# Kernel optimization log

Measured on AMD Instinct MI355X. Metric: run time of the kernel, lower is better.

## Reference

```python
import jax, jax.numpy as jnp
import numpy as np

N, E, D, H, L = 20000, 100000, 768, 8, 3
DH = D // H
WSCALE = 0.02  # small init so exp() in attention stays finite


def setup_inputs() -> dict:
    key = jax.random.key(0)
    ks = jax.random.split(key, 16)
    inp = {
        'x': jax.random.normal(ks[0], (N, D), jnp.float32),
        'edge_attr': jax.random.normal(ks[1], (E, D), jnp.float32),
        'Wck': jax.random.normal(ks[2], (L, 2 * D, D), jnp.float32) * WSCALE,
        'bck': jnp.zeros((L, D), jnp.float32),
        'Wq': jax.random.normal(ks[3], (L, D, D), jnp.float32) * WSCALE,
        'bq': jnp.zeros((L, D), jnp.float32),
        'Wv': jax.random.normal(ks[4], (L, D, D), jnp.float32) * WSCALE,
        'bv': jnp.zeros((L, D), jnp.float32),
        'Waw': jax.random.normal(ks[5], (L, H, H), jnp.float32) * WSCALE,
        'baw': jnp.zeros((L, H), jnp.float32),
        'Wc': jax.random.normal(ks[6], (L, D, D), jnp.float32) * WSCALE,
        'bc': jnp.zeros((L, D), jnp.float32),
        'Wlx': jax.random.normal(ks[7], (L, D, D), jnp.float32) * WSCALE,
        'blx': jnp.zeros((L, D), jnp.float32),
        'Wla1': jax.random.normal(ks[8], (L, 2 * D, D), jnp.float32) * WSCALE,
        'bla1': jnp.zeros((L, D), jnp.float32),
        'Wla2': jax.random.normal(ks[9], (L, D, 2), jnp.float32) * WSCALE,
        'bla2': jnp.zeros((L, 2), jnp.float32),
        'edge_index': jax.random.randint(ks[10], (2, E), 0, N, jnp.int64),
    }
    return inp


def _gnn_layer(x, edge_attr, src, dst, Wck, bck, Wq, bq, Wv, bv, Waw, baw,
               Wc, bc, Wlx, blx, Wla1, bla1, Wla2, bla2):
    n = x.shape[0]
    # per-edge query (target node) and key (edge_attr || source node)
    q = x[dst] @ Wq + bq                                        # [E, D]
    k = jnp.concatenate([edge_attr, x[src]], axis=1) @ Wck + bck  # [E, D]
    qh = q.reshape(-1, H, DH)
    kh = k.reshape(-1, H, DH)
    aw = jnp.einsum('ehd,ehd->eh', qh, kh) / jnp.sqrt(jnp.float32(D))  # [E, H]
    a = jnp.exp(jax.nn.leaky_relu(aw, 0.2) @ Waw + baw)          # [E, H]
    # GAT-style softmax normalization over incoming edges of each target node
    sc = jax.ops.segment_sum(a, dst, num_segments=n)             # [N, H]
    ad = sc[dst]
    ad = jnp.where(ad == 0, jnp.float32(1), ad)
    att = (a / ad)[:, :, None]                                   # [E, H, 1]
    # weighted message from source nodes, scattered to targets
    v = (x[src] @ Wv + bv).reshape(-1, H, DH)                    # [E, H, DH]
    msg = (att * v).reshape(-1, D) @ Wc + bc                     # [E, D]
    h = jax.ops.segment_sum(msg, dst, num_segments=n)            # [N, D]
    # sgnn gated residual combine
    lx = x @ Wlx + blx
    z = jax.nn.leaky_relu(jnp.concatenate([lx, h], axis=1) @ Wla1 + bla1, 0.2) @ Wla2 + bla2
    la = jax.nn.softmax(z, axis=1)                               # [N, 2]
    return x * la[:, 0:1] + h * la[:, 1:2]


def reference(x, edge_attr, Wck, bck, Wq, bq, Wv, bv, Waw, baw, Wc, bc,
              Wlx, blx, Wla1, bla1, Wla2, bla2, edge_index):
    src = edge_index[0]
    dst = edge_index[1]
    for l in range(L):
        x = _gnn_layer(x, edge_attr, src, dst,
                       Wck[l], bck[l], Wq[l], bq[l], Wv[l], bv[l],
                       Waw[l], baw[l], Wc[l], bc[l], Wlx[l], blx[l],
                       Wla1[l], bla1[l], Wla2[l], bla2[l])
    return x
```

## Files before the change

### kernel.cpp

```cpp
#include <hip/hip_runtime.h>
#include <hip/hip_bf16.h>
#include <math.h>

#define DD 768
#define HH 8
#define DHH 96
#define NL 3
#define NN 20000
#define EE 100000

typedef __attribute__((ext_vector_type(8))) __bf16 bf16x8;
typedef __attribute__((ext_vector_type(4))) float f32x4;
typedef __attribute__((ext_vector_type(8))) unsigned short u16x8;

__host__ __device__ static inline int imin(int a, int b) { return a < b ? a : b; }

__device__ inline float b2f(unsigned short u) {
    union { unsigned int v; float f; } x; x.v = ((unsigned int)u) << 16; return x.f;
}
__device__ inline unsigned short f2b_rne(float f) {
    union { float f; unsigned int v; } x; x.f = f;
    unsigned int v = x.v;
    return (unsigned short)((v + 0x7FFFu + ((v >> 16) & 1u)) >> 16);
}
__device__ inline void b2f2(unsigned int u, float& lo, float& hi) {
    union { unsigned int v; float f; } x;
    x.v = u << 16; lo = x.f;
    x.v = u & 0xffff0000u; hi = x.f;
}
__device__ inline unsigned int packbf(float a, float b) {
    return (unsigned int)f2b_rne(a) | ((unsigned int)f2b_rne(b) << 16);
}

__global__ void deg_kernel(const int* __restrict__ dst, int* __restrict__ cnt)
{
    int i = blockIdx.x * 256 + threadIdx.x;
    if (i < EE) atomicAdd(&cnt[dst[i]], 1);
}

__global__ __launch_bounds__(256)
void scan_kernel(const int* __restrict__ deg, int* __restrict__ rowptr, int* __restrict__ cursor)
{
    __shared__ int part[256];
    int t = threadIdx.x;
    const int per = (NN + 255) / 256;
    int lo = t * per, hi = imin(NN, lo + per);
    int s = 0;
    for (int i = lo; i < hi; i++) s += deg[i];
    part[t] = s;
    __syncthreads();
    if (t == 0) {
        int acc = 0;
        for (int i = 0; i < 256; i++) { int v = part[i]; part[i] = acc; acc += v; }
        rowptr[NN] = acc;
    }
    __syncthreads();
    int run = part[t];
    for (int i = lo; i < hi; i++) {
        rowptr[i] = run; cursor[i] = run;
        run += deg[i];
    }
}

__global__ void fill_perm(const int* __restrict__ src, const int* __restrict__ dst,
                          int* __restrict__ cursor, int* __restrict__ perm,
                          int* __restrict__ src_s)
{
    int e = blockIdx.x * 256 + threadIdx.x;
    if (e >= EE) return;
    int d = dst[e];
    int pos = atomicAdd(&cursor[d], 1);
    perm[pos] = e;
    src_s[pos] = src[e];
}

__global__ void degf_kernel(const int* __restrict__ rowptr, float* __restrict__ degf)
{
    int n = blockIdx.x * 256 + threadIdx.x;
    if (n < NN) degf[n] = (float)(rowptr[n + 1] - rowptr[n]);
}

__global__ void f2b_kernel(const float* __restrict__ in, unsigned short* __restrict__ out, int n8)
{
    int i = blockIdx.x * 256 + threadIdx.x;
    if (i >= n8) return;
    const float4* p = reinterpret_cast<const float4*>(in + (size_t)i * 8);
    float4 a = p[0], b = p[1];
    u16x8 o;
    o[0] = f2b_rne(a.x); o[1] = f2b_rne(a.y); o[2] = f2b_rne(a.z); o[3] = f2b_rne(a.w);
    o[4] = f2b_rne(b.x); o[5] = f2b_rne(b.y); o[6] = f2b_rne(b.z); o[7] = f2b_rne(b.w);
    *reinterpret_cast<u16x8*>(out + (size_t)i * 8) = o;
}

__global__ void f2b_gather(const float* __restrict__ in, const int* __restrict__ perm,
                           unsigned short* __restrict__ out)
{
    int i = blockIdx.x * 256 + threadIdx.x;
    if (i >= EE * 96) return;
    int m = i / 96;
    int d8 = (i % 96) * 8;
    int row = perm[m];
    const float4* p = reinterpret_cast<const float4*>(in + (size_t)row * DD + d8);
    float4 a = p[0], b = p[1];
    u16x8 o;
    o[0] = f2b_rne(a.x); o[1] = f2b_rne(a.y); o[2] = f2b_rne(a.z); o[3] = f2b_rne(a.w);
    o[4] = f2b_rne(b.x); o[5] = f2b_rne(b.y); o[6] = f2b_rne(b.z); o[7] = f2b_rne(b.w);
    *reinterpret_cast<u16x8*>(out + (size_t)m * DD + d8) = o;
}

__global__ void transpose_w(const float* __restrict__ W, unsigned short* __restrict__ Wt,
                            int Kin, int out_ld, int out_off,
                            size_t strideW, size_t strideWt)
{
    __shared__ float tile[32][33];
    int z = blockIdx.z;
    W  += (size_t)z * strideW;
    Wt += (size_t)z * strideWt;
    int kb = blockIdx.x * 32, nb = blockIdx.y * 32;
    int tx = threadIdx.x & 31, ty = threadIdx.x >> 5;
#pragma unroll
    for (int i = 0; i < 32; i += 8)
        tile[ty + i][tx] = W[(size_t)(kb + ty + i) * DD + nb + tx];
    __syncthreads();
#pragma unroll
    for (int i = 0; i < 32; i += 8)
        Wt[(size_t)(nb + ty + i) * out_ld + out_off + kb + tx] = f2b_rne(tile[tx][ty + i]);
}

__global__ void biasf_kernel(const float* __restrict__ blx, const float* __restrict__ Wla1,
                             const float* __restrict__ bla1, float* __restrict__ bf)
{
    int l = blockIdx.y;
    const float* blxl  = blx  + (size_t)l * DD;
    const float* Wla1l = Wla1 + (size_t)l * 2 * DD * DD;
    const float* bla1l = bla1 + (size_t)l * DD;
    float* bfl = bf + (size_t)l * DD;
    int n = blockIdx.x * 256 + threadIdx.x;
    if (n >= DD) return;
    float s = bla1l[n];
    for (int k = 0; k < DD; k++) s += blxl[k] * Wla1l[(size_t)k * DD + n];
    bfl[n] = s;
}

__global__ void biasqkv_kernel(const float* __restrict__ bq, const float* __restrict__ bv,
                               float* __restrict__ bqkv)
{
    int l = blockIdx.y;
    int i = blockIdx.x * 256 + threadIdx.x;
    if (i >= 3 * DD) return;
    float v = 0.f;
    if (i < DD) v = bq[(size_t)l * DD + i];
    else if (i >= 2 * DD) v = bv[(size_t)l * DD + i - 2 * DD];
    bqkv[(size_t)l * 3 * DD + i] = v;
}

__global__ __launch_bounds__(512, 2)
void gemm_mfma(const unsigned short* __restrict__ A0,
               const unsigned short* __restrict__ A1,
               const unsigned short* __restrict__ Wt,
               const float* __restrict__ bias,
               const float* __restrict__ rowscale,
               float* __restrict__ C32,
               unsigned short* __restrict__ C16,
               int M, int K, int Nw,
               size_t bsA, size_t bsW, size_t bsC)
{
    __shared__ __align__(16) char smem[98304];
    const int z = blockIdx.z;
    A0 += (size_t)z * bsA;
    Wt += (size_t)z * bsW;
    if (C32) C32 += (size_t)z * bsC;
    if (C16) C16 += (size_t)z * bsC;
    const int t = threadIdx.x;
    const int l = t & 63;
    const int w = t >> 6;
    const int wm = w & 3, wn = w >> 2;

    const int gx = gridDim.x;
    const int nwg = gx * gridDim.y;
    const int lin = blockIdx.y * gx + blockIdx.x;
    const int xcd = lin & 7, pos = lin >> 3;
    const int q8 = nwg >> 3, r8 = nwg & 7;
    const int base = (xcd < r8) ? xcd * (q8 + 1) : r8 * (q8 + 1) + (xcd - r8) * q8;
    const int swz = base + pos;
    const int bn = swz % gx, bm = swz / gx;

    const int srow = t >> 3;
    const int ssrc = ((t & 7) ^ (srow & 7)) * 8;

    const int lane_r = l & 15;
    const int lane_k = l >> 4;

    auto STAGE = [&](int buf, int k0) {
        char* As = smem + buf * 49152;
        char* Bs = As + 32768;
        const unsigned short* Ap; int kbase;
        if (k0 < DD) { Ap = A0; kbase = k0; }
        else         { Ap = A1; kbase = k0 - DD; }
#pragma unroll
        for (int i = 0; i < 4; i++) {
            int grow = bm * 256 + i * 64 + srow;
            if (grow >= M) grow = M - 1;
            char* ldstA = As + ((i * 64 + w * 8) << 7);
            const unsigned short* g = Ap + (size_t)grow * DD + kbase + ssrc;
            __builtin_amdgcn_global_load_lds(
                (const __attribute__((address_space(1))) void*)g,
                (__attribute__((address_space(3))) void*)ldstA, 16, 0, 0);
        }
#pragma unroll
        for (int i = 0; i < 2; i++) {
            int gn = bn * 128 + i * 64 + srow;
            const unsigned short* gB = Wt + (size_t)gn * K + k0 + ssrc;
            char* ldstB = Bs + ((i * 64 + w * 8) << 7);
            __builtin_amdgcn_global_load_lds(
                (const __attribute__((address_space(1))) void*)gB,
                (__attribute__((address_space(3))) void*)ldstB, 16, 0, 0);
        }
    };

    f32x4 acc[4][4];
#pragma unroll
    for (int m = 0; m < 4; m++)
#pragma unroll
        for (int n = 0; n < 4; n++) acc[m][n] = (f32x4){0.f, 0.f, 0.f, 0.f};

    const int nt = K >> 6;
    STAGE(0, 0);
    int cur = 0;
    for (int tt = 0; tt < nt; tt++) {
        if (tt + 1 < nt) {
            STAGE(cur ^ 1, (tt + 1) << 6);
            asm volatile("s_waitcnt vmcnt(6)" ::: "memory");
        } else {
            asm volatile("s_waitcnt vmcnt(0)" ::: "memory");
        }
        __builtin_amdgcn_s_barrier();
        __builtin_amdgcn_sched_barrier(0);
        char* As = smem + cur * 49152;
        char* Bs = As + 32768;
        __builtin_amdgcn_s_setprio(1);
#pragma unroll
        for (int kk = 0; kk < 2; kk++) {
            bf16x8 af[4], bfr[4];
#pragma unroll
            for (int m = 0; m < 4; m++) {
                int r = wm * 64 + m * 16 + lane_r;
                int slot = (kk * 4 + lane_k) ^ (r & 7);
                af[m] = *reinterpret_cast<const bf16x8*>(As + r * 128 + slot * 16);
            }
#pragma unroll
            for (int n = 0; n < 4; n++) {
                int r = wn * 64 + n * 16 + lane_r;
                int slot = (kk * 4 + lane_k) ^ (r & 7);
                bfr[n] = *reinterpret_cast<const bf16x8*>(Bs + r * 128 + slot * 16);
            }
#pragma unroll
            for (int m = 0; m < 4; m++)
#pragma unroll
                for (int n = 0; n < 4; n++)
                    acc[m][n] = __builtin_amdgcn_mfma_f32_16x16x32_bf16(
                        af[m], bfr[n], acc[m][n], 0, 0, 0);
        }
        __builtin_amdgcn_s_setprio(0);
        asm volatile("s_waitcnt lgkmcnt(0)" ::: "memory");
        __builtin_amdgcn_sched_barrier(0);
        __builtin_amdgcn_s_barrier();
        cur ^= 1;
    }

    if (C32) {
#pragma unroll
        for (int n = 0; n < 4; n++) {
            int col = bn * 128 + wn * 64 + n * 16 + lane_r;
            float badd = bias ? bias[col] : 0.f;
#pragma unroll
            for (int m = 0; m < 4; m++) {
#pragma unroll
                for (int j = 0; j < 4; j++) {
                    int r = bm * 256 + wm * 64 + m * 16 + lane_k * 4 + j;
                    if (r < M) {
                        float bs = rowscale ? rowscale[r] : 1.f;
                        C32[(size_t)r * Nw + col] = acc[m][n][j] + badd * bs;
                    }
                }
            }
        }
    }
    if (C16) {
        unsigned short* cs = (unsigned short*)smem;
#pragma unroll
        for (int n = 0; n < 4; n++) {
            int lcol = wn * 64 + n * 16 + lane_r;
            float badd = bias ? bias[bn * 128 + lcol] : 0.f;
#pragma unroll
            for (int m = 0; m < 4; m++) {
#pragma unroll
                for (int j = 0; j < 4; j++) {
                    int lr = wm * 64 + m * 16 + lane_k * 4 + j;
                    int r = bm * 256 + lr;
                    float bs = rowscale ? (r < M ? rowscale[r] : 0.f) : 1.f;
                    cs[lr * 136 + lcol] = f2b_rne(acc[m][n][j] + badd * bs);
                }
            }
        }
        __syncthreads();
        int rr = t >> 1, half = t & 1;
        int grow = bm * 256 + rr;
        if (grow < M) {
            u16x8* dst = reinterpret_cast<u16x8*>(C16 + (size_t)grow * Nw + bn * 128 + half * 64);
            const u16x8* s = reinterpret_cast<const u16x8*>(cs + rr * 136 + half * 64);
#pragma unroll
            for (int c = 0; c < 8; c++) dst[c] = s[c];
        }
    }
}

__global__ __launch_bounds__(128)
void edge_fused(const unsigned short* __restrict__ kea,
                const unsigned short* __restrict__ qkv,
                const float* __restrict__ Waw, const float* __restrict__ baw,
                const int* __restrict__ rowptr, const int* __restrict__ src_s,
                unsigned short* __restrict__ agg)
{
    __shared__ float awsh[HH];
    __shared__ float WawS[HH * HH];
    __shared__ float bawS[HH];
    const int n = blockIdx.x;
    const int t = threadIdx.x;
    const int d0 = t * 6;
    const int h = t >> 4;
    if (t < HH * HH) WawS[t] = Waw[t];
    if (t < HH) bawS[t] = baw[t];
    const int jlo = rowptr[n], jhi = rowptr[n + 1];
    const unsigned int* qr = reinterpret_cast<const unsigned int*>(qkv + (size_t)n * (3 * DD) + d0);
    float q[6];
    b2f2(qr[0], q[0], q[1]); b2f2(qr[1], q[2], q[3]); b2f2(qr[2], q[4], q[5]);
    float acc[6] = {0.f, 0.f, 0.f, 0.f, 0.f, 0.f};
    float sa = 0.f;
    constexpr float rs = 0.03608439182435161f;
    __syncthreads();
    for (int j = jlo; j < jhi; j++) {
        int s = src_s[j];
        const unsigned int* ke = reinterpret_cast<const unsigned int*>(kea + (size_t)j * DD + d0);
        const unsigned int* kr = reinterpret_cast<const unsigned int*>(qkv + (size_t)s * (3 * DD) + DD + d0);
        const unsigned int* vr = reinterpret_cast<const unsigned int*>(qkv + (size_t)s * (3 * DD) + 2 * DD + d0);
        float part = 0.f;
        float ka, kb2, va, vb;
#pragma unroll
        for (int c = 0; c < 3; c++) {
            b2f2(ke[c], ka, kb2);
            b2f2(kr[c], va, vb);
            part = fmaf(q[2 * c], ka + va, part);
            part = fmaf(q[2 * c + 1], kb2 + vb, part);
        }
        part += __shfl_xor(part, 1);
        part += __shfl_xor(part, 2);
        part += __shfl_xor(part, 4);
        part += __shfl_xor(part, 8);
        if ((t & 15) == 0) awsh[h] = part;
        __syncthreads();
        float zz = bawS[h];
#pragma unroll
        for (int h2 = 0; h2 < HH; h2++) {
            float aw = awsh[h2] * rs;
            float tt = aw > 0.f ? aw : 0.2f * aw;
            zz = fmaf(tt, WawS[h2 * HH + h], zz);
        }
        float a = expf(zz);
        sa += a;
        float v0, v1;
#pragma unroll
        for (int c = 0; c < 3; c++) {
            b2f2(vr[c], v0, v1);
            acc[2 * c]     = fmaf(a, v0, acc[2 * c]);
            acc[2 * c + 1] = fmaf(a, v1, acc[2 * c + 1]);
        }
        __syncthreads();
    }
    float inv = (sa == 0.f) ? 1.f : 1.f / sa;
    unsigned int* ag = reinterpret_cast<unsigned int*>(agg + (size_t)n * DD + d0);
    ag[0] = packbf(acc[0] * inv, acc[1] * inv);
    ag[1] = packbf(acc[2] * inv, acc[3] * inv);
    ag[2] = packbf(acc[4] * inv, acc[5] * inv);
}

__global__ __launch_bounds__(256)
void combine_kernel(const unsigned short* __restrict__ g, const float* __restrict__ Wla2,
                    const float* __restrict__ bla2, unsigned short* __restrict__ x16,
                    const unsigned short* __restrict__ h, float* __restrict__ outf, int Nn)
{
    int w = threadIdx.x >> 6;
    int lane = threadIdx.x & 63;
    int n = blockIdx.x * 4 + w;
    if (n >= Nn) return;
    float z0 = 0.f, z1 = 0.f;
#pragma unroll
    for (int p = 0; p < 3; p++) {
        int d = p * 256 + lane * 4;
        const unsigned short* gp = g + (size_t)n * DD + d;
#pragma unroll
        for (int j = 0; j < 4; j++) {
            float gv = b2f(gp[j]);
            float tt = gv > 0.f ? gv : 0.2f * gv;
            z0 = fmaf(tt, Wla2[(d + j) * 2 + 0], z0);
            z1 = fmaf(tt, Wla2[(d + j) * 2 + 1], z1);
        }
    }
#pragma unroll
    for (int off = 32; off > 0; off >>= 1) {
        z0 += __shfl_xor(z0, off);
        z1 += __shfl_xor(z1, off);
    }
    z0 += bla2[0]; z1 += bla2[1];
    float mx = fmaxf(z0, z1);
    float e0v = expf(z0 - mx), e1v = expf(z1 - mx);
    float inv = 1.f / (e0v + e1v);
    float la0 = e0v * inv, la1 = e1v * inv;
#pragma unroll
    for (int p = 0; p < 3; p++) {
        int d = p * 256 + lane * 4;
        unsigned short* xp = x16 + (size_t)n * DD + d;
        const unsigned short* hp = h + (size_t)n * DD + d;
        float o[4];
#pragma unroll
        for (int j = 0; j < 4; j++)
            o[j] = b2f(xp[j]) * la0 + b2f(hp[j]) * la1;
#pragma unroll
        for (int j = 0; j < 4; j++) xp[j] = f2b_rne(o[j]);
        if (outf) {
            float4 ov = make_float4(o[0], o[1], o[2], o[3]);
            *reinterpret_cast<float4*>((float*)outf + (size_t)n * DD + d) = ov;
        }
    }
}

extern "C" void kernel_launch(void* const* d_in, const int* in_sizes, int n_in,
                              void* d_out, int out_size, void* d_ws, size_t ws_size,
                              hipStream_t stream)
{
    const int N = NN, E = EE;
    const float* x_in      = (const float*)d_in[0];
    const float* edge_attr = (const float*)d_in[1];
    const float* Wck = (const float*)d_in[2];
    const float* bck = (const float*)d_in[3];
    const float* Wq  = (const float*)d_in[4];
    const float* bq  = (const float*)d_in[5];
    const float* Wv  = (const float*)d_in[6];
    const float* bv  = (const float*)d_in[7];
    const float* Waw = (const float*)d_in[8];
    const float* baw = (const float*)d_in[9];
    const float* Wc  = (const float*)d_in[10];
    const float* bc  = (const float*)d_in[11];
    const float* Wlx = (const float*)d_in[12];
    const float* blx = (const float*)d_in[13];
    const float* Wla1 = (const float*)d_in[14];
    const float* bla1 = (const float*)d_in[15];
    const float* Wla2 = (const float*)d_in[16];
    const float* bla2 = (const float*)d_in[17];
    const int* eidx = (const int*)d_in[18];
    const int* srcp = eidx;
    const int* dstp = eidx + E;

    const size_t DDDD = (size_t)DD * DD;
    float* p = (float*)d_ws;
    const size_t NB = (size_t)N * DD;
    float* degf  = p; p += N;
    float* wfx32 = p; p += NL * DDDD;
    float* bfbuf = p; p += NL * DD;
    float* bqkvb = p; p += NL * 3 * DD;
    int* rowptr = (int*)p;
    int* cursor = rowptr + (N + 1);
    int* perm   = cursor + N;
    int* src_s  = perm + E;
    p += (size_t)(2 * N + 1 + 2 * E + 63) / 64 * 64;
    unsigned short* xb16  = (unsigned short*)p; p += NB / 2;
    unsigned short* hb16  = (unsigned short*)p; p += NB / 2;
    unsigned short* agg16 = (unsigned short*)p; p += NB / 2;
    unsigned short* qkv16 = (unsigned short*)p; p += 3 * NB / 2;
    unsigned short* ea16  = (unsigned short*)p; p += (size_t)E * DD / 2;
    unsigned short* kea16 = (unsigned short*)p; p += (size_t)E * DD / 2;
    unsigned short* gb16  = qkv16;
    unsigned short* wqkvt  = (unsigned short*)p; p += NL * 3 * DDDD / 2;
    unsigned short* wcktopt= (unsigned short*)p; p += NL * DDDD / 2;
    unsigned short* wct    = (unsigned short*)p; p += NL * DDDD / 2;
    unsigned short* wla1tt = (unsigned short*)p; p += NL * DDDD / 2;
    unsigned short* wst3   = (unsigned short*)p; p += NL * 2 * DDDD / 2;
    unsigned short* wlx16  = (unsigned short*)p; p += NL * DDDD / 2;

    hipMemsetAsync(cursor, 0, N * sizeof(int), stream);
    deg_kernel<<<(E + 255) / 256, 256, 0, stream>>>(dstp, cursor);
    scan_kernel<<<1, 256, 0, stream>>>(cursor, rowptr, cursor);
    fill_perm<<<(E + 255) / 256, 256, 0, stream>>>(srcp, dstp, cursor, perm, src_s);
    degf_kernel<<<(N + 255) / 256, 256, 0, stream>>>(rowptr, degf);
    f2b_gather<<<(E * 96 + 255) / 256, 256, 0, stream>>>(edge_attr, perm, ea16);
    f2b_kernel<<<(N * 96 + 255) / 256, 256, 0, stream>>>(x_in, xb16, N * 96);

    dim3 gt3(DD / 32, DD / 32, NL);
    transpose_w<<<gt3, 256, 0, stream>>>(Wq, wqkvt, DD, DD, 0, DDDD, 3 * DDDD);
    transpose_w<<<gt3, 256, 0, stream>>>(Wck + DDDD, wqkvt + DDDD, DD, DD, 0, 2 * DDDD, 3 * DDDD);
    transpose_w<<<gt3, 256, 0, stream>>>(Wv, wqkvt + 2 * DDDD, DD, DD, 0, DDDD, 3 * DDDD);
    transpose_w<<<gt3, 256, 0, stream>>>(Wck, wcktopt, DD, DD, 0, 2 * DDDD, DDDD);
    transpose_w<<<gt3, 256, 0, stream>>>(Wc, wct, DD, DD, 0, DDDD, DDDD);
    transpose_w<<<gt3, 256, 0, stream>>>(Wla1, wla1tt, DD, DD, 0, 2 * DDDD, DDDD);
    transpose_w<<<gt3, 256, 0, stream>>>(Wla1 + DDDD, wst3, DD, 2 * DD, DD, 2 * DDDD, 2 * DDDD);
    f2b_kernel<<<(NL * DD * 96 + 255) / 256, 256, 0, stream>>>(Wlx, wlx16, NL * DD * 96);
    gemm_mfma<<<dim3(6, 3, NL), 512, 0, stream>>>(wlx16, nullptr, wla1tt, nullptr, nullptr,
                                                  wfx32, nullptr, DD, DD, DD,
                                                  DDDD, DDDD, DDDD);
    transpose_w<<<gt3, 256, 0, stream>>>(wfx32, wst3, DD, 2 * DD, 0, DDDD, 2 * DDDD);
    biasf_kernel<<<dim3(3, NL), 256, 0, stream>>>(blx, Wla1, bla1, bfbuf);
    biasqkv_kernel<<<dim3(9, NL), 256, 0, stream>>>(bq, bv, bqkvb);

    for (int l = 0; l < NL; l++) {
        const float* bck_l = bck + (size_t)l * DD;
        const float* Waw_l = Waw + (size_t)l * HH * HH;
        const float* baw_l = baw + (size_t)l * HH;
        const float* bc_l  = bc  + (size_t)l * DD;
        const float* Wla2_l = Wla2 + (size_t)l * DD * 2;
        const float* bla2_l = bla2 + (size_t)l * 2;

        gemm_mfma<<<dim3(18, (N + 255) / 256), 512, 0, stream>>>(
            xb16, nullptr, wqkvt + (size_t)l * 3 * DDDD, bqkvb + (size_t)l * 3 * DD,
            nullptr, nullptr, qkv16, N, DD, 3 * DD, 0, 0, 0);
        gemm_mfma<<<dim3(6, (E + 255) / 256), 512, 0, stream>>>(
            ea16, nullptr, wcktopt + (size_t)l * DDDD, bck_l,
            nullptr, nullptr, kea16, E, DD, DD, 0, 0, 0);
        edge_fused<<<N, 128, 0, stream>>>(kea16, qkv16, Waw_l, baw_l, rowptr, src_s, agg16);
        gemm_mfma<<<dim3(6, (N + 255) / 256), 512, 0, stream>>>(
            agg16, nullptr, wct + (size_t)l * DDDD, bc_l,
            degf, nullptr, hb16, N, DD, DD, 0, 0, 0);
        gemm_mfma<<<dim3(6, (N + 255) / 256), 512, 0, stream>>>(
            xb16, hb16, wst3 + (size_t)l * 2 * DDDD, bfbuf + (size_t)l * DD,
            nullptr, nullptr, gb16, N, 2 * DD, DD, 0, 0, 0);
        combine_kernel<<<(N + 3) / 4, 256, 0, stream>>>(
            gb16, Wla2_l, bla2_l, xb16, hb16,
            (l == NL - 1) ? (float*)d_out : nullptr, N);
    }
}
```

Baseline: 1.954 ms.

## Enlarge GEMM tiles to 256x256 with interleaved quarter-tile staged prefetch

Measured after the change: 1.913 ms. -2.1%, faster.

```diff
diff --git a/kernel.cpp b/kernel.cpp
--- a/kernel.cpp
+++ b/kernel.cpp
@@ -154,7 +154,7 @@
     bqkv[(size_t)l * 3 * DD + i] = v;
 }
 
-__global__ __launch_bounds__(512, 2)
+__global__ __launch_bounds__(512, 1)
 void gemm_mfma(const unsigned short* __restrict__ A0,
                const unsigned short* __restrict__ A1,
                const unsigned short* __restrict__ Wt,
@@ -165,7 +165,7 @@
                int M, int K, int Nw,
                size_t bsA, size_t bsW, size_t bsC)
 {
-    __shared__ __align__(16) char smem[98304];
+    __shared__ __align__(16) char smem[131072];
     const int z = blockIdx.z;
     A0 += (size_t)z * bsA;
     Wt += (size_t)z * bsW;
@@ -174,7 +174,8 @@
     const int t = threadIdx.x;
     const int l = t & 63;
     const int w = t >> 6;
-    const int wm = w & 3, wn = w >> 2;
+    const int wm = w >> 2;
+    const int wn = w & 3;
 
     const int gx = gridDim.x;
     const int nwg = gx * gridDim.y;
@@ -191,77 +192,143 @@
     const int lane_r = l & 15;
     const int lane_k = l >> 4;
 
-    auto STAGE = [&](int buf, int k0) {
-        char* As = smem + buf * 49152;
-        char* Bs = As + 32768;
+    auto STAGE_A2 = [&](int buf, int k0, int i0) {
+        char* As_ = smem + buf * 65536;
         const unsigned short* Ap; int kbase;
         if (k0 < DD) { Ap = A0; kbase = k0; }
         else         { Ap = A1; kbase = k0 - DD; }
 #pragma unroll
-        for (int i = 0; i < 4; i++) {
+        for (int i = i0; i < i0 + 2; i++) {
             int grow = bm * 256 + i * 64 + srow;
             if (grow >= M) grow = M - 1;
-            char* ldstA = As + ((i * 64 + w * 8) << 7);
             const unsigned short* g = Ap + (size_t)grow * DD + kbase + ssrc;
             __builtin_amdgcn_global_load_lds(
                 (const __attribute__((address_space(1))) void*)g,
-                (__attribute__((address_space(3))) void*)ldstA, 16, 0, 0);
-        }
-#pragma unroll
-        for (int i = 0; i < 2; i++) {
-            int gn = bn * 128 + i * 64 + srow;
-            const unsigned short* gB = Wt + (size_t)gn * K + k0 + ssrc;
-            char* ldstB = Bs + ((i * 64 + w * 8) << 7);
+                (__attribute__((address_space(3))) void*)(As_ + ((i * 64 + w * 8) << 7)),
+                16, 0, 0);
+        }
+    };
+    auto STAGE_B2 = [&](int buf, int k0, int i0) {
+        char* Bs_ = smem + buf * 65536 + 32768;
+#pragma unroll
+        for (int i = i0; i < i0 + 2; i++) {
+            int gn = bn * 256 + i * 64 + srow;
+            const unsigned short* g = Wt + (size_t)gn * K + k0 + ssrc;
             __builtin_amdgcn_global_load_lds(
-                (const __attribute__((address_space(1))) void*)gB,
-                (__attribute__((address_space(3))) void*)ldstB, 16, 0, 0);
+                (const __attribute__((address_space(1))) void*)g,
+                (__attribute__((address_space(3))) void*)(Bs_ + ((i * 64 + w * 8) << 7)),
+                16, 0, 0);
         }
     };
 
-    f32x4 acc[4][4];
-#pragma unroll
-    for (int m = 0; m < 4; m++)
+    f32x4 acc[8][4];
+#pragma unroll
+    for (int m = 0; m < 8; m++)
 #pragma unroll
         for (int n = 0; n < 4; n++) acc[m][n] = (f32x4){0.f, 0.f, 0.f, 0.f};
 
     const int nt = K >> 6;
-    STAGE(0, 0);
+    STAGE_A2(0, 0, 0); STAGE_A2(0, 0, 2);
+    STAGE_B2(0, 0, 0); STAGE_B2(0, 0, 2);
     int cur = 0;
+
     for (int tt = 0; tt < nt; tt++) {
-        if (tt + 1 < nt) {
-            STAGE(cur ^ 1, (tt + 1) << 6);
-            asm volatile("s_waitcnt vmcnt(6)" ::: "memory");
+        const bool pre = (tt + 1 < nt);
+        const int nk0 = (tt + 1) << 6;
+        char* As = smem + cur * 65536;
+        char* Bs = As + 32768;
+        bf16x8 bfr[4];
+
+        if (pre) {
+            STAGE_A2(cur ^ 1, nk0, 0);
+            asm volatile("s_waitcnt vmcnt(2)" ::: "memory");
         } else {
             asm volatile("s_waitcnt vmcnt(0)" ::: "memory");
         }
         __builtin_amdgcn_s_barrier();
         __builtin_amdgcn_sched_barrier(0);
-        char* As = smem + cur * 49152;
-        char* Bs = As + 32768;
-        __builtin_amdgcn_s_setprio(1);
-#pragma unroll
-        for (int kk = 0; kk < 2; kk++) {
-            bf16x8 af[4], bfr[4];
+#pragma unroll
+        for (int n = 0; n < 4; n++) {
+            int r = wn * 64 + n * 16 + lane_r;
+            int slot = lane_k ^ (r & 7);
+            bfr[n] = *reinterpret_cast<const bf16x8*>(Bs + r * 128 + slot * 16);
+        }
+        {
+            bf16x8 af[4];
 #pragma unroll
             for (int m = 0; m < 4; m++) {
-                int r = wm * 64 + m * 16 + lane_r;
-                int slot = (kk * 4 + lane_k) ^ (r & 7);
+                int r = wm * 128 + m * 16 + lane_r;
+                int slot = lane_k ^ (r & 7);
                 af[m] = *reinterpret_cast<const bf16x8*>(As + r * 128 + slot * 16);
             }
-#pragma unroll
-            for (int n = 0; n < 4; n++) {
-                int r = wn * 64 + n * 16 + lane_r;
-                int slot = (kk * 4 + lane_k) ^ (r & 7);
-                bfr[n] = *reinterpret_cast<const bf16x8*>(Bs + r * 128 + slot * 16);
+            __builtin_amdgcn_s_setprio(1);
+#pragma unroll
+            for (int m = 0; m < 4; m++)
+#pragma unroll
+                for (int n = 0; n < 4; n++)
+                    acc[m][n] = __builtin_amdgcn_mfma_f32_16x16x32_bf16(af[m], bfr[n], acc[m][n], 0, 0, 0);
+            __builtin_amdgcn_s_setprio(0);
+        }
+        if (pre) STAGE_A2(cur ^ 1, nk0, 2);
+        __builtin_amdgcn_s_barrier();
+        {
+            bf16x8 af[4];
+#pragma unroll
+            for (int m = 0; m < 4; m++) {
+                int r = wm * 128 + (4 + m) * 16 + lane_r;
+                int slot = lane_k ^ (r & 7);
+                af[m] = *reinterpret_cast<const bf16x8*>(As + r * 128 + slot * 16);
             }
+            __builtin_amdgcn_s_setprio(1);
 #pragma unroll
             for (int m = 0; m < 4; m++)
 #pragma unroll
                 for (int n = 0; n < 4; n++)
-                    acc[m][n] = __builtin_amdgcn_mfma_f32_16x16x32_bf16(
-                        af[m], bfr[n], acc[m][n], 0, 0, 0);
-        }
-        __builtin_amdgcn_s_setprio(0);
+                    acc[4 + m][n] = __builtin_amdgcn_mfma_f32_16x16x32_bf16(af[m], bfr[n], acc[4 + m][n], 0, 0, 0);
+            __builtin_amdgcn_s_setprio(0);
+        }
+        if (pre) STAGE_B2(cur ^ 1, nk0, 0);
+        __builtin_amdgcn_s_barrier();
+#pragma unroll
+        for (int n = 0; n < 4; n++) {
+            int r = wn * 64 + n * 16 + lane_r;
+            int slot = (4 + lane_k) ^ (r & 7);
+            bfr[n] = *reinterpret_cast<const bf16x8*>(Bs + r * 128 + slot * 16);
+        }
+        {
+            bf16x8 af[4];
+#pragma unroll
+            for (int m = 0; m < 4; m++) {
+                int r = wm * 128 + m * 16 + lane_r;
+                int slot = (4 + lane_k) ^ (r & 7);
+                af[m] = *reinterpret_cast<const bf16x8*>(As + r * 128 + slot * 16);
+            }
+            __builtin_amdgcn_s_setprio(1);
+#pragma unroll
+            for (int m = 0; m < 4; m++)
+#pragma unroll
+                for (int n = 0; n < 4; n++)
+                    acc[m][n] = __builtin_amdgcn_mfma_f32_16x16x32_bf16(af[m], bfr[n], acc[m][n], 0, 0, 0);
+            __builtin_amdgcn_s_setprio(0);
+        }
+        if (pre) STAGE_B2(cur ^ 1, nk0, 2);
+        __builtin_amdgcn_s_barrier();
+        {
+            bf16x8 af[4];
+#pragma unroll
+            for (int m = 0; m < 4; m++) {
+                int r = wm * 128 + (4 + m) * 16 + lane_r;
+                int slot = (4 + lane_k) ^ (r & 7);
+                af[m] = *reinterpret_cast<const bf16x8*>(As + r * 128 + slot * 16);
+            }
+            __builtin_amdgcn_s_setprio(1);
+#pragma unroll
+            for (int m = 0; m < 4; m++)
+#pragma unroll
+                for (int n = 0; n < 4; n++)
+                    acc[4 + m][n] = __builtin_amdgcn_mfma_f32_16x16x32_bf16(af[m], bfr[n], acc[4 + m][n], 0, 0, 0);
+            __builtin_amdgcn_s_setprio(0);
+        }
         asm volatile("s_waitcnt lgkmcnt(0)" ::: "memory");
         __builtin_amdgcn_sched_barrier(0);
         __builtin_amdgcn_s_barrier();
@@ -271,13 +338,13 @@
     if (C32) {
 #pragma unroll
         for (int n = 0; n < 4; n++) {
-            int col = bn * 128 + wn * 64 + n * 16 + lane_r;
+            int col = bn * 256 + wn * 64 + n * 16 + lane_r;
             float badd = bias ? bias[col] : 0.f;
 #pragma unroll
-            for (int m = 0; m < 4; m++) {
+            for (int m = 0; m < 8; m++) {
 #pragma unroll
                 for (int j = 0; j < 4; j++) {
-                    int r = bm * 256 + wm * 64 + m * 16 + lane_k * 4 + j;
+                    int r = bm * 256 + wm * 128 + m * 16 + lane_k * 4 + j;
                     if (r < M) {
                         float bs = rowscale ? rowscale[r] : 1.f;
                         C32[(size_t)r * Nw + col] = acc[m][n][j] + badd * bs;
@@ -289,28 +356,34 @@
     if (C16) {
         unsigned short* cs = (unsigned short*)smem;
 #pragma unroll
-        for (int n = 0; n < 4; n++) {
-            int lcol = wn * 64 + n * 16 + lane_r;
-            float badd = bias ? bias[bn * 128 + lcol] : 0.f;
-#pragma unroll
-            for (int m = 0; m < 4; m++) {
-#pragma unroll
-                for (int j = 0; j < 4; j++) {
-                    int lr = wm * 64 + m * 16 + lane_k * 4 + j;
-                    int r = bm * 256 + lr;
-                    float bs = rowscale ? (r < M ? rowscale[r] : 0.f) : 1.f;
-                    cs[lr * 136 + lcol] = f2b_rne(acc[m][n][j] + badd * bs);
+        for (int half = 0; half < 2; half++) {
+            __syncthreads();
+            if (wm == half) {
+#pragma unroll
+                for (int n = 0; n < 4; n++) {
+                    int lcol = wn * 64 + n * 16 + lane_r;
+                    float badd = bias ? bias[bn * 256 + lcol] : 0.f;
+#pragma unroll
+                    for (int m = 0; m < 8; m++) {
+#pragma unroll
+                        for (int j = 0; j < 4; j++) {
+                            int lr = m * 16 + lane_k * 4 + j;
+                            int r = bm * 256 + half * 128 + lr;
+                            float bs = rowscale ? (r < M ? rowscale[r] : 0.f) : 1.f;
+                            cs[lr * 264 + lcol] = f2b_rne(acc[m][n][j] + badd * bs);
+                        }
+                    }
                 }
             }
-        }
-        __syncthreads();
-        int rr = t >> 1, half = t & 1;
-        int grow = bm * 256 + rr;
-        if (grow < M) {
-            u16x8* dst = reinterpret_cast<u16x8*>(C16 + (size_t)grow * Nw + bn * 128 + half * 64);
-            const u16x8* s = reinterpret_cast<const u16x8*>(cs + rr * 136 + half * 64);
-#pragma unroll
-            for (int c = 0; c < 8; c++) dst[c] = s[c];
+            __syncthreads();
+            int rr = t >> 2, qd = (t & 3) * 64;
+            int grow = bm * 256 + half * 128 + rr;
+            if (grow < M) {
+                u16x8* dst = reinterpret_cast<u16x8*>(C16 + (size_t)grow * Nw + bn * 256 + qd);
+                const u16x8* s = reinterpret_cast<const u16x8*>(cs + rr * 264 + qd);
+#pragma unroll
+                for (int c = 0; c < 8; c++) dst[c] = s[c];
+            }
         }
     }
 }
@@ -504,7 +577,7 @@
     transpose_w<<<gt3, 256, 0, stream>>>(Wla1, wla1tt, DD, DD, 0, 2 * DDDD, DDDD);
     transpose_w<<<gt3, 256, 0, stream>>>(Wla1 + DDDD, wst3, DD, 2 * DD, DD, 2 * DDDD, 2 * DDDD);
     f2b_kernel<<<(NL * DD * 96 + 255) / 256, 256, 0, stream>>>(Wlx, wlx16, NL * DD * 96);
-    gemm_mfma<<<dim3(6, 3, NL), 512, 0, stream>>>(wlx16, nullptr, wla1tt, nullptr, nullptr,
+    gemm_mfma<<<dim3(3, 3, NL), 512, 0, stream>>>(wlx16, nullptr, wla1tt, nullptr, nullptr,
                                                   wfx32, nullptr, DD, DD, DD,
                                                   DDDD, DDDD, DDDD);
     transpose_w<<<gt3, 256, 0, stream>>>(wfx32, wst3, DD, 2 * DD, 0, DDDD, 2 * DDDD);
@@ -519,17 +592,17 @@
         const float* Wla2_l = Wla2 + (size_t)l * DD * 2;
         const float* bla2_l = bla2 + (size_t)l * 2;
 
-        gemm_mfma<<<dim3(18, (N + 255) / 256), 512, 0, stream>>>(
+        gemm_mfma<<<dim3(9, (N + 255) / 256), 512, 0, stream>>>(
             xb16, nullptr, wqkvt + (size_t)l * 3 * DDDD, bqkvb + (size_t)l * 3 * DD,
             nullptr, nullptr, qkv16, N, DD, 3 * DD, 0, 0, 0);
-        gemm_mfma<<<dim3(6, (E + 255) / 256), 512, 0, stream>>>(
+        gemm_mfma<<<dim3(3, (E + 255) / 256), 512, 0, stream>>>(
             ea16, nullptr, wcktopt + (size_t)l * DDDD, bck_l,
             nullptr, nullptr, kea16, E, DD, DD, 0, 0, 0);
         edge_fused<<<N, 128, 0, stream>>>(kea16, qkv16, Waw_l, baw_l, rowptr, src_s, agg16);
-        gemm_mfma<<<dim3(6, (N + 255) / 256), 512, 0, stream>>>(
+        gemm_mfma<<<dim3(3, (N + 255) / 256), 512, 0, stream>>>(
             agg16, nullptr, wct + (size_t)l * DDDD, bc_l,
             degf, nullptr, hb16, N, DD, DD, 0, 0, 0);
-        gemm_mfma<<<dim3(6, (N + 255) / 256), 512, 0, stream>>>(
+        gemm_mfma<<<dim3(3, (N + 255) / 256), 512, 0, stream>>>(
             xb16, hb16, wst3 + (size_t)l * 2 * DDDD, bfbuf + (size_t)l * DD,
             nullptr, nullptr, gb16, N, 2 * DD, DD, 0, 0, 0);
         combine_kernel<<<(N + 3) / 4, 256, 0, stream>>>(
```
